# Kernel tuning notes

Measured on AMD Instinct MI355X. Metric: run time of the kernel, lower is better.

Reference implementation:

```python
import jax, jax.numpy as jnp
import numpy as np

C_IN = 256
C_HIDDEN = 64
NO_HEADS = 8
INF = 1e9
EPS = 1e-10
B, R, N = 1, 256, 2048  # batch, N_res, N_seq


def setup_inputs() -> dict:
    key = jax.random.key(0)
    ks = jax.random.split(key, 9)
    m = jax.random.normal(ks[0], (B, R, N, C_IN), dtype=jnp.float32)
    mask = (jax.random.uniform(ks[1], (B, R, N)) > 0.1).astype(jnp.float32)
    s = 0.02
    Wq = jax.random.normal(ks[2], (C_IN, C_HIDDEN * NO_HEADS), dtype=jnp.float32) * s
    Wk = jax.random.normal(ks[3], (C_IN, C_HIDDEN), dtype=jnp.float32) * s
    Wv = jax.random.normal(ks[4], (C_IN, C_HIDDEN), dtype=jnp.float32) * s
    Wg = jax.random.normal(ks[5], (C_IN, C_HIDDEN * NO_HEADS), dtype=jnp.float32) * s
    bg = jax.random.normal(ks[6], (C_HIDDEN * NO_HEADS,), dtype=jnp.float32) * s
    Wo = jax.random.normal(ks[7], (C_HIDDEN * NO_HEADS, C_IN), dtype=jnp.float32) * s
    bo = jax.random.normal(ks[8], (C_IN,), dtype=jnp.float32) * s
    return {"m": m, "mask": mask, "Wq": Wq, "Wk": Wk, "Wv": Wv,
            "Wg": Wg, "bg": bg, "Wo": Wo, "bo": bo}


def reference(m, mask, Wq, Wk, Wv, Wg, bg, Wo, bo):
    # masked-mean pooled global query: [B, R, c_in]
    q = jnp.sum(m * mask[..., None], axis=-2) / (jnp.sum(mask, axis=-1)[..., None] + EPS)
    q = (q @ Wq) * (C_HIDDEN ** -0.5)                      # [B, R, H*c]
    q = q.reshape(q.shape[:-1] + (NO_HEADS, C_HIDDEN))    # [B, R, H, c]
    k = m @ Wk                                             # [B, R, N, c]
    v = m @ Wv                                             # [B, R, N, c]
    bias = INF * (mask - 1.0)                              # [B, R, N]
    a = jnp.einsum('brhc,brnc->brhn', q, k) + bias[..., None, :]
    a = jax.nn.softmax(a, axis=-1)                         # [B, R, H, N]
    o = jnp.einsum('brhn,brnc->brhc', a, v)                # [B, R, H, c]
    g = jax.nn.sigmoid(m @ Wg + bg)                        # [B, R, N, H*c]
    g = g.reshape(g.shape[:-1] + (NO_HEADS, C_HIDDEN))     # [B, R, N, H, c]
    o = o[..., None, :, :] * g                             # [B, R, N, H, c]
    o = o.reshape(o.shape[:-2] + (NO_HEADS * C_HIDDEN,))   # [B, R, N, H*c]
    return o @ Wo + bo                                     # [B, R, N, c_in]
```

## Files before the change

### kernel.cpp

```cpp
#include <hip/hip_runtime.h>

#define RDIM 256
#define NDIM 2048
#define CI 256
#define CH 64
#define NH 8
#define HC 512

typedef short bfrag __attribute__((ext_vector_type(8)));
typedef float ffrag __attribute__((ext_vector_type(4)));
typedef float f32x4 __attribute__((ext_vector_type(4)));
typedef unsigned short u16x4 __attribute__((ext_vector_type(4)));
typedef unsigned short u16x8 __attribute__((ext_vector_type(8)));

#define MFMA16 __builtin_amdgcn_mfma_f32_16x16x32_bf16

__device__ __forceinline__ unsigned short f2bf(float f) {
  union { float f; unsigned u; } v; v.f = f;
  unsigned r = v.u + 0x7fffu + ((v.u >> 16) & 1u);
  return (unsigned short)(r >> 16);
}

__global__ __launch_bounds__(256) void k0_prep(
    const float* __restrict__ Wk, const float* __restrict__ Wv,
    const float* __restrict__ Wg, const float* __restrict__ Wo,
    unsigned short* __restrict__ wkf, unsigned short* __restrict__ wvf,
    unsigned short* __restrict__ wgf, unsigned short* __restrict__ wof,
    float* __restrict__ qsum, float* __restrict__ msum) {
  const int tid = blockIdx.x * 256 + threadIdx.x;
  const int nth = gridDim.x * 256;
  for (int i = tid; i < RDIM * CI; i += nth) qsum[i] = 0.f;
  for (int i = tid; i < RDIM; i += nth) msum[i] = 0.f;
  for (int i = tid; i < 16384; i += nth) {
    int j = i & 7, l = (i >> 3) & 63, ks = (i >> 9) & 7, ct = i >> 12;
    int k = ks * 32 + (l >> 4) * 8 + j, c = ct * 16 + (l & 15);
    wkf[i] = f2bf(Wk[k * 64 + c]);
    wvf[i] = f2bf(Wv[k * 64 + c]);
  }
  for (int i = tid; i < 131072; i += nth) {
    int j = i & 7, l = (i >> 3) & 63, ks = (i >> 9) & 7, ct = i >> 12;
    int k = ks * 32 + (l >> 4) * 8 + j, c = ct * 16 + (l & 15);
    wgf[i] = f2bf(Wg[k * 512 + c]);
  }
  for (int i = tid; i < 131072; i += nth) {
    int j = i & 7, l = (i >> 3) & 63, ks = (i >> 9) & 15, ct = i >> 13;
    int k = ks * 32 + (l >> 4) * 8 + j, co = ct * 16 + (l & 15);
    wof[i] = f2bf(Wo[k * 256 + co]);
  }
}

__global__ __launch_bounds__(256) void k1_proj(
    const float* __restrict__ m, const float* __restrict__ mask,
    const unsigned short* __restrict__ wkf, const unsigned short* __restrict__ wvf,
    float* __restrict__ qsum, float* __restrict__ msum,
    unsigned short* __restrict__ kbuf, unsigned short* __restrict__ vbuf) {
  const int r = blockIdx.x >> 4;
  const int nb = (blockIdx.x & 15) << 7;
  const int t = threadIdx.x;
  const int lane = t & 63, w = t >> 6;
  __shared__ float msk[128];
  if (t < 128) msk[t] = mask[r * NDIM + nb + t];
  __syncthreads();
  {
    const float* mp = m + ((size_t)r * NDIM + nb) * CI + t;
    float s = 0.f;
#pragma unroll 8
    for (int i = 0; i < 128; ++i) s += mp[(size_t)i * CI] * msk[i];
    atomicAdd(&qsum[r * CI + t], s);
    if (t < 128) {
      float v = msk[t];
#pragma unroll
      for (int o = 32; o; o >>= 1) v += __shfl_down(v, o);
      if (lane == 0) atomicAdd(&msum[r], v);
    }
  }
  ffrag ak[4][2], av[4][2];
  const ffrag z = {0.f, 0.f, 0.f, 0.f};
#pragma unroll
  for (int ct = 0; ct < 4; ++ct)
#pragma unroll
    for (int st = 0; st < 2; ++st) { ak[ct][st] = z; av[ct][st] = z; }
  const int row0 = nb + w * 32;
  const float* mbase = m + ((size_t)r * NDIM + row0 + (lane & 15)) * CI + (lane >> 4) * 8;
  for (int ks = 0; ks < 8; ++ks) {
    bfrag mf[2];
#pragma unroll
    for (int st = 0; st < 2; ++st) {
      const f32x4* p = (const f32x4*)(mbase + (size_t)st * 16 * CI + ks * 32);
      f32x4 x = p[0], y = p[1];
      bfrag q;
      q[0] = (short)f2bf(x[0]); q[1] = (short)f2bf(x[1]);
      q[2] = (short)f2bf(x[2]); q[3] = (short)f2bf(x[3]);
      q[4] = (short)f2bf(y[0]); q[5] = (short)f2bf(y[1]);
      q[6] = (short)f2bf(y[2]); q[7] = (short)f2bf(y[3]);
      mf[st] = q;
    }
#pragma unroll
    for (int ct = 0; ct < 4; ++ct) {
      bfrag wk = *(const bfrag*)(wkf + (((ct * 8 + ks) * 64 + lane) << 3));
      bfrag wv = *(const bfrag*)(wvf + (((ct * 8 + ks) * 64 + lane) << 3));
#pragma unroll
      for (int st = 0; st < 2; ++st) {
        ak[ct][st] = MFMA16(wk, mf[st], ak[ct][st], 0, 0, 0);
        av[ct][st] = MFMA16(mf[st], wv, av[ct][st], 0, 0, 0);
      }
    }
  }
#pragma unroll
  for (int ct = 0; ct < 4; ++ct)
#pragma unroll
    for (int st = 0; st < 2; ++st) {
      u16x4 pk, pv;
#pragma unroll
      for (int q = 0; q < 4; ++q) { pk[q] = f2bf(ak[ct][st][q]); pv[q] = f2bf(av[ct][st][q]); }
      int nk = row0 + st * 16 + (lane & 15);
      int ck = ct * 16 + (lane >> 4) * 4;
      *(u16x4*)(kbuf + ((size_t)r * NDIM + nk) * CH + ck) = pk;
      int nv = row0 + st * 16 + (lane >> 4) * 4;
      int cv = ct * 16 + (lane & 15);
      *(u16x4*)(vbuf + ((size_t)r * CH + cv) * NDIM + nv) = pv;
    }
}

__global__ __launch_bounds__(512) void k2_attn(
    const float* __restrict__ mask, const float* __restrict__ Wq,
    const float* __restrict__ qsum, const float* __restrict__ msum,
    const unsigned short* __restrict__ kbuf, const unsigned short* __restrict__ vbuf,
    float* __restrict__ ows) {
  const int r = blockIdx.x;
  const int t = threadIdx.x, lane = t & 63, w = t >> 6;
  __shared__ float qs[256];
  __shared__ float ql[16][64];
  __shared__ float al[8][2048];
  __shared__ unsigned short pl[16 * 2048];
  __shared__ float rden[8];
  if (t < 256) qs[t] = qsum[r * CI + t];
  __syncthreads();
  const float inv = 1.f / (msum[r] + 1e-10f);
  {
    float s = 0.f;
    for (int ci = 0; ci < 256; ++ci) s += qs[ci] * Wq[ci * HC + t];
    ql[t >> 6][t & 63] = s * inv * 0.125f;
    ql[8 + (t >> 6)][t & 63] = 0.f;
  }
  __syncthreads();
  bfrag qf[2];
#pragma unroll
  for (int kq = 0; kq < 2; ++kq)
#pragma unroll
    for (int j = 0; j < 8; ++j)
      qf[kq][j] = (short)f2bf(ql[lane & 15][kq * 32 + (lane >> 4) * 8 + j]);
  for (int ch = w; ch < 128; ch += 8) {
    int n0 = ch << 4;
    ffrag d = {0.f, 0.f, 0.f, 0.f};
#pragma unroll
    for (int kq = 0; kq < 2; ++kq) {
      bfrag kf = *(const bfrag*)(kbuf + ((size_t)r * NDIM + n0 + (lane & 15)) * CH +
                                 kq * 32 + (lane >> 4) * 8);
      d = MFMA16(qf[kq], kf, d, 0, 0, 0);
    }
    float b = 1e9f * (mask[r * NDIM + n0 + (lane & 15)] - 1.f);
    if ((lane >> 4) < 2) {
#pragma unroll
      for (int q = 0; q < 4; ++q)
        al[(lane >> 4) * 4 + q][n0 + (lane & 15)] = d[q] + b;
    }
  }
  __syncthreads();
  {
    const int h = w;
    float mx = -3.0e38f;
    for (int i = lane; i < 2048; i += 64) mx = fmaxf(mx, al[h][i]);
#pragma unroll
    for (int o = 32; o; o >>= 1) mx = fmaxf(mx, __shfl_xor(mx, o));
    float sum = 0.f;
    for (int i = lane; i < 2048; i += 64) {
      float e = __expf(al[h][i] - mx);
      sum += e;
      int byte = (h * 4096 + i * 2) ^ ((h & 7) << 4);
      *(unsigned short*)((char*)pl + byte) = f2bf(e);
    }
#pragma unroll
    for (int o = 32; o; o >>= 1) sum += __shfl_xor(sum, o);
    if (lane == 0) rden[h] = 1.f / sum;
    const int h2 = 8 + w;
    for (int i = lane; i < 2048; i += 64) {
      int byte = (h2 * 4096 + i * 2) ^ ((h2 & 7) << 4);
      *(unsigned short*)((char*)pl + byte) = 0;
    }
  }
  __syncthreads();
  if (w < 4) {
    ffrag acc = {0.f, 0.f, 0.f, 0.f};
    const int c0 = w << 4;
    for (int ks = 0; ks < 64; ++ks) {
      int hh = lane & 15;
      int byte = (hh * 4096 + (ks * 32 + (lane >> 4) * 8) * 2) ^ ((hh & 7) << 4);
      bfrag pf = *(const bfrag*)((char*)pl + byte);
      bfrag vf = *(const bfrag*)(vbuf + ((size_t)r * CH + c0 + (lane & 15)) * NDIM +
                                 ks * 32 + (lane >> 4) * 8);
      acc = MFMA16(pf, vf, acc, 0, 0, 0);
    }
    if ((lane >> 4) < 2) {
#pragma unroll
      for (int q = 0; q < 4; ++q) {
        int h = (lane >> 4) * 4 + q;
        ows[r * HC + h * CH + c0 + (lane & 15)] = acc[q] * rden[h];
      }
    }
  }
}

__global__ __launch_bounds__(512) void k3_out(
    const float* __restrict__ m, const unsigned short* __restrict__ wgf,
    const unsigned short* __restrict__ wof, const float* __restrict__ bg,
    const float* __restrict__ bo, const float* __restrict__ ows,
    float* __restrict__ out) {
  const int r = blockIdx.x >> 4;
  const int nb = (blockIdx.x & 15) << 7;
  const int t = threadIdx.x;
  const int lane = t & 63, w = t >> 6;
  __shared__ unsigned short ml[128 * 256];
  __shared__ unsigned short actl[64 * 512];
  __shared__ float ogl[512], bgl[512], bol[256];
  ogl[t] = ows[r * HC + t];
  bgl[t] = bg[t];
  if (t < 256) bol[t] = bo[t];
  for (int ch = t; ch < 4096; ch += 512) {
    int n = ch >> 5;
    int c8 = (ch & 31) * 8;
    const f32x4* p = (const f32x4*)(m + ((size_t)r * NDIM + nb + n) * CI + c8);
    f32x4 x = p[0], y = p[1];
    u16x8 pk;
    pk[0] = f2bf(x[0]); pk[1] = f2bf(x[1]); pk[2] = f2bf(x[2]); pk[3] = f2bf(x[3]);
    pk[4] = f2bf(y[0]); pk[5] = f2bf(y[1]); pk[6] = f2bf(y[2]); pk[7] = f2bf(y[3]);
    int byte = (n * 512 + c8 * 2) ^ ((n & 7) << 4);
    *(u16x8*)((char*)ml + byte) = pk;
  }
  __syncthreads();
  const ffrag z = {0.f, 0.f, 0.f, 0.f};
  for (int half = 0; half < 2; ++half) {
    ffrag acc1[4][4];
#pragma unroll
    for (int a = 0; a < 4; ++a)
#pragma unroll
      for (int b = 0; b < 4; ++b) acc1[a][b] = z;
    for (int ks = 0; ks < 8; ++ks) {
      bfrag bf[4];
#pragma unroll
      for (int nt = 0; nt < 4; ++nt) {
        int n = half * 64 + nt * 16 + (lane & 15);
        int byte = (n * 512 + (ks * 32 + (lane >> 4) * 8) * 2) ^ ((n & 7) << 4);
        bf[nt] = *(const bfrag*)((char*)ml + byte);
      }
#pragma unroll
      for (int t4 = 0; t4 < 4; ++t4) {
        int ct = w * 4 + t4;
        bfrag a = *(const bfrag*)(wgf + (((ct * 8 + ks) * 64 + lane) << 3));
#pragma unroll
        for (int nt = 0; nt < 4; ++nt)
          acc1[t4][nt] = MFMA16(a, bf[nt], acc1[t4][nt], 0, 0, 0);
      }
    }
    __syncthreads();
#pragma unroll
    for (int t4 = 0; t4 < 4; ++t4)
#pragma unroll
      for (int nt = 0; nt < 4; ++nt) {
        int hc0 = (w * 4 + t4) * 16 + (lane >> 4) * 4;
        int n = nt * 16 + (lane & 15);
        u16x4 pk;
#pragma unroll
        for (int q = 0; q < 4; ++q) {
          float gl = acc1[t4][nt][q] + bgl[hc0 + q];
          float g = 1.f / (1.f + __expf(-gl));
          pk[q] = f2bf(g * ogl[hc0 + q]);
        }
        int byte = (n * 1024 + hc0 * 2) ^ ((n & 7) << 4);
        *(u16x4*)((char*)actl + byte) = pk;
      }
    __syncthreads();
    ffrag acc2[2][4];
#pragma unroll
    for (int a = 0; a < 2; ++a)
#pragma unroll
      for (int b = 0; b < 4; ++b) acc2[a][b] = z;
    for (int ks = 0; ks < 16; ++ks) {
      bfrag bf[4];
#pragma unroll
      for (int nt = 0; nt < 4; ++nt) {
        int n = nt * 16 + (lane & 15);
        int byte = (n * 1024 + (ks * 32 + (lane >> 4) * 8) * 2) ^ ((n & 7) << 4);
        bf[nt] = *(const bfrag*)((char*)actl + byte);
      }
#pragma unroll
      for (int t2 = 0; t2 < 2; ++t2) {
        int ct = w * 2 + t2;
        bfrag a = *(const bfrag*)(wof + (((ct * 16 + ks) * 64 + lane) << 3));
#pragma unroll
        for (int nt = 0; nt < 4; ++nt)
          acc2[t2][nt] = MFMA16(a, bf[nt], acc2[t2][nt], 0, 0, 0);
      }
    }
#pragma unroll
    for (int t2 = 0; t2 < 2; ++t2)
#pragma unroll
      for (int nt = 0; nt < 4; ++nt) {
        int co0 = (w * 2 + t2) * 16 + (lane >> 4) * 4;
        int n = nb + half * 64 + nt * 16 + (lane & 15);
        f32x4 o;
#pragma unroll
        for (int q = 0; q < 4; ++q) o[q] = acc2[t2][nt][q] + bol[co0 + q];
        *(f32x4*)(out + ((size_t)r * NDIM + n) * CI + co0) = o;
      }
  }
}

extern "C" void kernel_launch(void* const* d_in, const int* in_sizes, int n_in,
                              void* d_out, int out_size, void* d_ws, size_t ws_size,
                              hipStream_t stream) {
  const float* m    = (const float*)d_in[0];
  const float* mask = (const float*)d_in[1];
  const float* Wq   = (const float*)d_in[2];
  const float* Wk   = (const float*)d_in[3];
  const float* Wv   = (const float*)d_in[4];
  const float* Wg   = (const float*)d_in[5];
  const float* bg   = (const float*)d_in[6];
  const float* Wo   = (const float*)d_in[7];
  const float* bo   = (const float*)d_in[8];
  float* out = (float*)d_out;
  char* ws = (char*)d_ws;
  unsigned short* wkf  = (unsigned short*)(ws);
  unsigned short* wvf  = (unsigned short*)(ws + 32768);
  unsigned short* wgf  = (unsigned short*)(ws + 65536);
  unsigned short* wof  = (unsigned short*)(ws + 327680);
  float*          qsum = (float*)(ws + 589824);
  float*          msum = (float*)(ws + 851968);
  float*          ows  = (float*)(ws + 852992);
  unsigned short* kbuf = (unsigned short*)(ws + 1377280);
  unsigned short* vbuf = (unsigned short*)(ws + 68486144);

  hipLaunchKernelGGL(k0_prep, dim3(256), dim3(256), 0, stream,
                     Wk, Wv, Wg, Wo, wkf, wvf, wgf, wof, qsum, msum);
  hipLaunchKernelGGL(k1_proj, dim3(4096), dim3(256), 0, stream,
                     m, mask, wkf, wvf, qsum, msum, kbuf, vbuf);
  hipLaunchKernelGGL(k2_attn, dim3(256), dim3(512), 0, stream,
                     mask, Wq, qsum, msum, kbuf, vbuf, ows);
  hipLaunchKernelGGL(k3_out, dim3(4096), dim3(512), 0, stream,
                     m, wgf, wof, bg, bo, ows, out);
}
```

Measured before the change: 2.483 ms.

## Fuse masked pooling into projection loads and shrink k3 LDS for occupancy

Measured after the change: 3.549 ms. 1.43x slower.

```diff
diff --git a/kernel.cpp b/kernel.cpp
--- a/kernel.cpp
+++ b/kernel.cpp
@@ -49,7 +49,7 @@
   }
 }
 
-__global__ __launch_bounds__(256) void k1_proj(
+__global__ __launch_bounds__(256, 4) void k1_proj(
     const float* __restrict__ m, const float* __restrict__ mask,
     const unsigned short* __restrict__ wkf, const unsigned short* __restrict__ wvf,
     float* __restrict__ qsum, float* __restrict__ msum,
@@ -59,20 +59,15 @@
   const int t = threadIdx.x;
   const int lane = t & 63, w = t >> 6;
   __shared__ float msk[128];
+  __shared__ float pl[256];
   if (t < 128) msk[t] = mask[r * NDIM + nb + t];
-  __syncthreads();
-  {
-    const float* mp = m + ((size_t)r * NDIM + nb) * CI + t;
-    float s = 0.f;
-#pragma unroll 8
-    for (int i = 0; i < 128; ++i) s += mp[(size_t)i * CI] * msk[i];
-    atomicAdd(&qsum[r * CI + t], s);
-    if (t < 128) {
-      float v = msk[t];
-#pragma unroll
-      for (int o = 32; o; o >>= 1) v += __shfl_down(v, o);
-      if (lane == 0) atomicAdd(&msum[r], v);
-    }
+  pl[t] = 0.f;
+  __syncthreads();
+  if (t < 128) {
+    float v = msk[t];
+#pragma unroll
+    for (int o = 32; o; o >>= 1) v += __shfl_down(v, o);
+    if (lane == 0) atomicAdd(&msum[r], v);
   }
   ffrag ak[4][2], av[4][2];
   const ffrag z = {0.f, 0.f, 0.f, 0.f};
@@ -81,13 +76,21 @@
 #pragma unroll
     for (int st = 0; st < 2; ++st) { ak[ct][st] = z; av[ct][st] = z; }
   const int row0 = nb + w * 32;
+  const float wm0 = msk[w * 32 + (lane & 15)];
+  const float wm1 = msk[w * 32 + 16 + (lane & 15)];
   const float* mbase = m + ((size_t)r * NDIM + row0 + (lane & 15)) * CI + (lane >> 4) * 8;
   for (int ks = 0; ks < 8; ++ks) {
     bfrag mf[2];
+    float t8[8];
+#pragma unroll
+    for (int j = 0; j < 8; ++j) t8[j] = 0.f;
 #pragma unroll
     for (int st = 0; st < 2; ++st) {
       const f32x4* p = (const f32x4*)(mbase + (size_t)st * 16 * CI + ks * 32);
       f32x4 x = p[0], y = p[1];
+      const float wm = st ? wm1 : wm0;
+      t8[0] += x[0] * wm; t8[1] += x[1] * wm; t8[2] += x[2] * wm; t8[3] += x[3] * wm;
+      t8[4] += y[0] * wm; t8[5] += y[1] * wm; t8[6] += y[2] * wm; t8[7] += y[3] * wm;
       bfrag q;
       q[0] = (short)f2bf(x[0]); q[1] = (short)f2bf(x[1]);
       q[2] = (short)f2bf(x[2]); q[3] = (short)f2bf(x[3]);
@@ -104,6 +107,15 @@
         ak[ct][st] = MFMA16(wk, mf[st], ak[ct][st], 0, 0, 0);
         av[ct][st] = MFMA16(mf[st], wv, av[ct][st], 0, 0, 0);
       }
+    }
+#pragma unroll
+    for (int o = 1; o < 16; o <<= 1)
+#pragma unroll
+      for (int j = 0; j < 8; ++j) t8[j] += __shfl_xor(t8[j], o);
+    if ((lane & 15) == 0) {
+      const int c0 = ks * 32 + (lane >> 4) * 8;
+#pragma unroll
+      for (int j = 0; j < 8; ++j) atomicAdd(&pl[c0 + j], t8[j]);
     }
   }
 #pragma unroll
@@ -120,6 +132,8 @@
       int cv = ct * 16 + (lane & 15);
       *(u16x4*)(vbuf + ((size_t)r * CH + cv) * NDIM + nv) = pv;
     }
+  __syncthreads();
+  atomicAdd(&qsum[r * CI + t], pl[t]);
 }
 
 __global__ __launch_bounds__(512) void k2_attn(
@@ -211,7 +225,7 @@
   }
 }
 
-__global__ __launch_bounds__(512) void k3_out(
+__global__ __launch_bounds__(512, 4) void k3_out(
     const float* __restrict__ m, const unsigned short* __restrict__ wgf,
     const unsigned short* __restrict__ wof, const float* __restrict__ bg,
     const float* __restrict__ bo, const float* __restrict__ ows,
@@ -220,26 +234,26 @@
   const int nb = (blockIdx.x & 15) << 7;
   const int t = threadIdx.x;
   const int lane = t & 63, w = t >> 6;
-  __shared__ unsigned short ml[128 * 256];
-  __shared__ unsigned short actl[64 * 512];
+  __shared__ unsigned short ml[64 * 256];
+  __shared__ unsigned short actl[32 * 512];
   __shared__ float ogl[512], bgl[512], bol[256];
   ogl[t] = ows[r * HC + t];
   bgl[t] = bg[t];
   if (t < 256) bol[t] = bo[t];
-  for (int ch = t; ch < 4096; ch += 512) {
-    int n = ch >> 5;
-    int c8 = (ch & 31) * 8;
-    const f32x4* p = (const f32x4*)(m + ((size_t)r * NDIM + nb + n) * CI + c8);
-    f32x4 x = p[0], y = p[1];
-    u16x8 pk;
-    pk[0] = f2bf(x[0]); pk[1] = f2bf(x[1]); pk[2] = f2bf(x[2]); pk[3] = f2bf(x[3]);
-    pk[4] = f2bf(y[0]); pk[5] = f2bf(y[1]); pk[6] = f2bf(y[2]); pk[7] = f2bf(y[3]);
-    int byte = (n * 512 + c8 * 2) ^ ((n & 7) << 4);
-    *(u16x8*)((char*)ml + byte) = pk;
-  }
-  __syncthreads();
   const ffrag z = {0.f, 0.f, 0.f, 0.f};
-  for (int half = 0; half < 2; ++half) {
+  for (int h = 0; h < 2; ++h) {
+    for (int ch = t; ch < 2048; ch += 512) {
+      int n = ch >> 5;
+      int c8 = (ch & 31) * 8;
+      const f32x4* p = (const f32x4*)(m + ((size_t)r * NDIM + nb + h * 64 + n) * CI + c8);
+      f32x4 x = p[0], y = p[1];
+      u16x8 pk;
+      pk[0] = f2bf(x[0]); pk[1] = f2bf(x[1]); pk[2] = f2bf(x[2]); pk[3] = f2bf(x[3]);
+      pk[4] = f2bf(y[0]); pk[5] = f2bf(y[1]); pk[6] = f2bf(y[2]); pk[7] = f2bf(y[3]);
+      int byte = (n * 512 + c8 * 2) ^ ((n & 7) << 4);
+      *(u16x8*)((char*)ml + byte) = pk;
+    }
+    __syncthreads();
     ffrag acc1[4][4];
 #pragma unroll
     for (int a = 0; a < 4; ++a)
@@ -249,8 +263,8 @@
       bfrag bf[4];
 #pragma unroll
       for (int nt = 0; nt < 4; ++nt) {
-        int n = half * 64 + nt * 16 + (lane & 15);
-        int byte = (n * 512 + (ks * 32 + (lane >> 4) * 8) * 2) ^ ((n & 7) << 4);
+        int n = nt * 16 + (lane & 15);
+        int byte = (n * 512 + (ks * 64 + (lane >> 4) * 16)) ^ ((n & 7) << 4);
         bf[nt] = *(const bfrag*)((char*)ml + byte);
       }
 #pragma unroll
@@ -262,57 +276,59 @@
           acc1[t4][nt] = MFMA16(a, bf[nt], acc1[t4][nt], 0, 0, 0);
       }
     }
-    __syncthreads();
-#pragma unroll
-    for (int t4 = 0; t4 < 4; ++t4)
-#pragma unroll
-      for (int nt = 0; nt < 4; ++nt) {
-        int hc0 = (w * 4 + t4) * 16 + (lane >> 4) * 4;
-        int n = nt * 16 + (lane & 15);
-        u16x4 pk;
-#pragma unroll
-        for (int q = 0; q < 4; ++q) {
-          float gl = acc1[t4][nt][q] + bgl[hc0 + q];
-          float g = 1.f / (1.f + __expf(-gl));
-          pk[q] = f2bf(g * ogl[hc0 + q]);
+    for (int c2 = 0; c2 < 2; ++c2) {
+      __syncthreads();
+#pragma unroll
+      for (int t4 = 0; t4 < 4; ++t4)
+#pragma unroll
+        for (int ntc = 0; ntc < 2; ++ntc) {
+          int hc0 = (w * 4 + t4) * 16 + (lane >> 4) * 4;
+          int n32 = ntc * 16 + (lane & 15);
+          u16x4 pk;
+#pragma unroll
+          for (int q = 0; q < 4; ++q) {
+            float gl = acc1[t4][c2 * 2 + ntc][q] + bgl[hc0 + q];
+            float g = 1.f / (1.f + __expf(-gl));
+            pk[q] = f2bf(g * ogl[hc0 + q]);
+          }
+          int byte = (n32 * 1024 + hc0 * 2) ^ ((n32 & 7) << 4);
+          *(u16x4*)((char*)actl + byte) = pk;
         }
-        int byte = (n * 1024 + hc0 * 2) ^ ((n & 7) << 4);
-        *(u16x4*)((char*)actl + byte) = pk;
-      }
-    __syncthreads();
-    ffrag acc2[2][4];
-#pragma unroll
-    for (int a = 0; a < 2; ++a)
-#pragma unroll
-      for (int b = 0; b < 4; ++b) acc2[a][b] = z;
-    for (int ks = 0; ks < 16; ++ks) {
-      bfrag bf[4];
-#pragma unroll
-      for (int nt = 0; nt < 4; ++nt) {
-        int n = nt * 16 + (lane & 15);
-        int byte = (n * 1024 + (ks * 32 + (lane >> 4) * 8) * 2) ^ ((n & 7) << 4);
-        bf[nt] = *(const bfrag*)((char*)actl + byte);
-      }
-#pragma unroll
-      for (int t2 = 0; t2 < 2; ++t2) {
-        int ct = w * 2 + t2;
-        bfrag a = *(const bfrag*)(wof + (((ct * 16 + ks) * 64 + lane) << 3));
-#pragma unroll
-        for (int nt = 0; nt < 4; ++nt)
-          acc2[t2][nt] = MFMA16(a, bf[nt], acc2[t2][nt], 0, 0, 0);
-      }
-    }
-#pragma unroll
-    for (int t2 = 0; t2 < 2; ++t2)
-#pragma unroll
-      for (int nt = 0; nt < 4; ++nt) {
-        int co0 = (w * 2 + t2) * 16 + (lane >> 4) * 4;
-        int n = nb + half * 64 + nt * 16 + (lane & 15);
-        f32x4 o;
-#pragma unroll
-        for (int q = 0; q < 4; ++q) o[q] = acc2[t2][nt][q] + bol[co0 + q];
-        *(f32x4*)(out + ((size_t)r * NDIM + n) * CI + co0) = o;
-      }
+      __syncthreads();
+      ffrag acc2[2][2];
+#pragma unroll
+      for (int a = 0; a < 2; ++a)
+#pragma unroll
+        for (int b = 0; b < 2; ++b) acc2[a][b] = z;
+      for (int ks = 0; ks < 16; ++ks) {
+        bfrag bf[2];
+#pragma unroll
+        for (int ntc = 0; ntc < 2; ++ntc) {
+          int n32 = ntc * 16 + (lane & 15);
+          int byte = (n32 * 1024 + (ks * 64 + (lane >> 4) * 16)) ^ ((n32 & 7) << 4);
+          bf[ntc] = *(const bfrag*)((char*)actl + byte);
+        }
+#pragma unroll
+        for (int t2 = 0; t2 < 2; ++t2) {
+          int ct = w * 2 + t2;
+          bfrag a = *(const bfrag*)(wof + (((ct * 16 + ks) * 64 + lane) << 3));
+#pragma unroll
+          for (int ntc = 0; ntc < 2; ++ntc)
+            acc2[t2][ntc] = MFMA16(a, bf[ntc], acc2[t2][ntc], 0, 0, 0);
+        }
+      }
+#pragma unroll
+      for (int t2 = 0; t2 < 2; ++t2)
+#pragma unroll
+        for (int ntc = 0; ntc < 2; ++ntc) {
+          int co0 = (w * 2 + t2) * 16 + (lane >> 4) * 4;
+          int n = nb + h * 64 + c2 * 32 + ntc * 16 + (lane & 15);
+          f32x4 o;
+#pragma unroll
+          for (int q = 0; q < 4; ++q) o[q] = acc2[t2][ntc][q] + bol[co0 + q];
+          *(f32x4*)(out + ((size_t)r * NDIM + n) * CI + co0) = o;
+        }
+    }
   }
 }
 
```
